# Kernel tuning notes

Measured on AMD Instinct MI355X. Metric: run time of the kernel, lower is better.

## Reference

```python
import jax, jax.numpy as jnp
import numpy as np

B, S, H, P2 = 64, 512, 768, 46  # batch, seq, hidden, num_p*2


def setup_inputs() -> dict:
    key = jax.random.key(0)
    k1, k2, k3, k4 = jax.random.split(key, 4)
    hidden_states = jax.random.normal(k1, (B, S, H), dtype=jnp.float32)
    # subject start/end indices must lie within the valid (masked-in) prefix
    lengths = jax.random.randint(k2, (B,), S // 4, S + 1)  # cue lengths per sample
    input_mask = (jnp.arange(S)[None, :] < lengths[:, None]).astype(jnp.int32)
    ids = jax.random.randint(k3, (B, 2), 0, S // 4)
    batch_subject_ids = jnp.sort(ids, axis=1).astype(jnp.int32)
    W = jax.random.normal(k4, (P2, H), dtype=jnp.float32) * (1.0 / np.sqrt(H))
    b = jnp.zeros((P2,), dtype=jnp.float32)
    return {"hidden_states": hidden_states, "batch_subject_ids": batch_subject_ids,
            "input_mask": input_mask, "W": W, "b": b}


def reference(hidden_states, batch_subject_ids, input_mask, W, b):
    # per-sample subject embedding: h[b, start] + h[b, end]  -> [B, H]
    batch_idx = jnp.arange(hidden_states.shape[0])
    s = (hidden_states[batch_idx, batch_subject_ids[:, 0]]
         + hidden_states[batch_idx, batch_subject_ids[:, 1]])
    # broadcast-add s to the first cue_len positions of each sample
    cue_len = jnp.sum(input_mask, axis=1)  # [B]
    pos_mask = (jnp.arange(hidden_states.shape[1])[None, :] < cue_len[:, None])  # [B, S]
    h = hidden_states + s[:, None, :] * pos_mask[:, :, None].astype(hidden_states.dtype)
    # linear + sigmoid^4 (dropout is identity in eval mode)
    logits = jnp.einsum('bsh,ph->bsp', h, W) + b
    return jax.nn.sigmoid(logits) ** 4
```

## Files before the change

### kernel.cpp

```cpp
#include <hip/hip_runtime.h>

#define SEQ 512
#define HID 768
#define P2  46
#define BLK 256
#define KH  384
#define WST 392

typedef short bf16x8 __attribute__((ext_vector_type(8)));
typedef float f32x4  __attribute__((ext_vector_type(4)));

__device__ __forceinline__ unsigned short f2bf(float f) {
  union { float f; unsigned int u; } v; v.f = f;
  return (unsigned short)((v.u + 0x7FFFu + ((v.u >> 16) & 1u)) >> 16);
}

__global__ __launch_bounds__(64) void qk_kernel(const float* __restrict__ h,
                                                const int* __restrict__ ids,
                                                const float* __restrict__ W,
                                                float* __restrict__ q) {
  int b = blockIdx.x, p = blockIdx.y;
  int lane = threadIdx.x;
  int i0 = ids[b * 2 + 0], i1 = ids[b * 2 + 1];
  const float* r0 = h + ((size_t)b * SEQ + i0) * HID;
  const float* r1 = h + ((size_t)b * SEQ + i1) * HID;
  const float* w  = W + (size_t)p * HID;
  float acc = 0.f;
  #pragma unroll
  for (int j = 0; j < HID / 64; ++j) {
    int k = lane + j * 64;
    acc += (r0[k] + r1[k]) * w[k];
  }
  #pragma unroll
  for (int off = 32; off > 0; off >>= 1)
    acc += __shfl_down(acc, off, 64);
  if (lane == 0) q[b * P2 + p] = acc;
}

__global__ __launch_bounds__(BLK) void gemm_kernel(const float* __restrict__ h,
                                                   const int* __restrict__ mask,
                                                   const float* __restrict__ W,
                                                   const float* __restrict__ bias,
                                                   const float* __restrict__ q,
                                                   float* __restrict__ out) {
  __shared__ __align__(16) unsigned short wlds[48 * WST];

  const int tid  = threadIdx.x;
  const int lane = tid & 63, wv = tid >> 6;
  const int mr   = lane & 15, qd = lane >> 4;
  const int row0 = blockIdx.x * 64;
  const int b    = row0 >> 9;
  const int rowa = row0 + (wv << 4) + mr;
  const float* hrow = h + (size_t)rowa * HID + (qd << 3);

  f32x4 acc[3];
  #pragma unroll
  for (int nt = 0; nt < 3; ++nt) acc[nt] = f32x4{0.f, 0.f, 0.f, 0.f};

  auto stageW = [&](int half) {
    for (int i = tid; i < (2 * WST) / 2; i += BLK)
      ((unsigned int*)(wlds + 46 * WST))[i] = 0u;
    for (int i = tid; i < (P2 * KH) / 4; i += BLK) {
      int f = i * 4;
      int r = f / KH;
      int c = f - r * KH;
      float4 w4 = *(const float4*)(W + (size_t)r * HID + half * KH + c);
      ushort4 v;
      v.x = f2bf(w4.x); v.y = f2bf(w4.y); v.z = f2bf(w4.z); v.w = f2bf(w4.w);
      *(ushort4*)&wlds[r * WST + c] = v;
    }
  };

  auto phase = [&](int half) {
    const float* hb = hrow + half * KH;
    float4 abuf[24];
    #pragma unroll
    for (int i = 0; i < 24; ++i)
      abuf[i] = *(const float4*)(hb + (i >> 1) * 32 + (i & 1) * 4);
    #pragma unroll
    for (int it = 0; it < 12; ++it) {
      bf16x8 a;
      {
        float4 x0 = abuf[2 * it], x1 = abuf[2 * it + 1];
        a[0] = (short)f2bf(x0.x); a[1] = (short)f2bf(x0.y);
        a[2] = (short)f2bf(x0.z); a[3] = (short)f2bf(x0.w);
        a[4] = (short)f2bf(x1.x); a[5] = (short)f2bf(x1.y);
        a[6] = (short)f2bf(x1.z); a[7] = (short)f2bf(x1.w);
      }
      #pragma unroll
      for (int nt = 0; nt < 3; ++nt) {
        bf16x8 bb = *(const bf16x8*)&wlds[((nt << 4) + mr) * WST + it * 32 + (qd << 3)];
        acc[nt] = __builtin_amdgcn_mfma_f32_16x16x32_bf16(a, bb, acc[nt], 0, 0, 0);
      }
    }
  };

  stageW(0);
  __syncthreads();
  phase(0);
  __syncthreads();
  stageW(1);
  __syncthreads();
  phase(1);

  int mrow[4];
  #pragma unroll
  for (int i = 0; i < 4; ++i)
    mrow[i] = mask[row0 + (wv << 4) + (qd << 2) + i];

  #pragma unroll
  for (int nt = 0; nt < 3; ++nt) {
    int p = (nt << 4) + mr;
    if (p < P2) {
      float bv = bias[p];
      float qv = q[b * P2 + p];
      #pragma unroll
      for (int i = 0; i < 4; ++i) {
        int row = row0 + (wv << 4) + (qd << 2) + i;
        float x = acc[nt][i] + bv + (mrow[i] ? qv : 0.f);
        float sg = 1.f / (1.f + __expf(-x));
        sg *= sg; sg *= sg;
        out[(size_t)row * P2 + p] = sg;
      }
    }
  }
}

extern "C" void kernel_launch(void* const* d_in, const int* in_sizes, int n_in,
                              void* d_out, int out_size, void* d_ws, size_t ws_size,
                              hipStream_t stream) {
  const float* h    = (const float*)d_in[0];
  const int*   ids  = (const int*)d_in[1];
  const int*   mask = (const int*)d_in[2];
  const float* W    = (const float*)d_in[3];
  const float* bias = (const float*)d_in[4];
  float* out = (float*)d_out;
  float* q   = (float*)d_ws;

  qk_kernel<<<dim3(64, P2), 64, 0, stream>>>(h, ids, W, q);
  gemm_kernel<<<dim3((64 * SEQ) / 64), BLK, 0, stream>>>(h, mask, W, bias, q, out);
}
```

Measured before the change: 168.0 us.

## Fuse subject-projection kernel into GEMM and stage full W once in LDS

The separate qk kernel is removed. Each GEMM block now recomputes the per-sample subject projection q (s·W) itself, using LDS and a 4-lane reduction, so one launch and the global round-trip for q go away. The full 768-wide bf16 W is staged into LDS in a single pass, which drops the two-phase staging and its extra barriers. In exchange, all 512 blocks redo the q dot products and the W conversion, and LDS use roughly doubles to about 75KB per block, which may lower occupancy.

Measured after the change: 179.7 us. +6.9%, slower.

```diff
diff --git a/kernel.cpp b/kernel.cpp
--- a/kernel.cpp
+++ b/kernel.cpp
@@ -4,8 +4,7 @@
 #define HID 768
 #define P2  46
 #define BLK 256
-#define KH  384
-#define WST 392
+#define WST 776
 
 typedef short bf16x8 __attribute__((ext_vector_type(8)));
 typedef float f32x4  __attribute__((ext_vector_type(4)));
@@ -15,35 +14,15 @@
   return (unsigned short)((v.u + 0x7FFFu + ((v.u >> 16) & 1u)) >> 16);
 }
 
-__global__ __launch_bounds__(64) void qk_kernel(const float* __restrict__ h,
-                                                const int* __restrict__ ids,
-                                                const float* __restrict__ W,
-                                                float* __restrict__ q) {
-  int b = blockIdx.x, p = blockIdx.y;
-  int lane = threadIdx.x;
-  int i0 = ids[b * 2 + 0], i1 = ids[b * 2 + 1];
-  const float* r0 = h + ((size_t)b * SEQ + i0) * HID;
-  const float* r1 = h + ((size_t)b * SEQ + i1) * HID;
-  const float* w  = W + (size_t)p * HID;
-  float acc = 0.f;
-  #pragma unroll
-  for (int j = 0; j < HID / 64; ++j) {
-    int k = lane + j * 64;
-    acc += (r0[k] + r1[k]) * w[k];
-  }
-  #pragma unroll
-  for (int off = 32; off > 0; off >>= 1)
-    acc += __shfl_down(acc, off, 64);
-  if (lane == 0) q[b * P2 + p] = acc;
-}
-
-__global__ __launch_bounds__(BLK) void gemm_kernel(const float* __restrict__ h,
-                                                   const int* __restrict__ mask,
-                                                   const float* __restrict__ W,
-                                                   const float* __restrict__ bias,
-                                                   const float* __restrict__ q,
-                                                   float* __restrict__ out) {
+__global__ __launch_bounds__(BLK) void fused_kernel(const float* __restrict__ h,
+                                                    const int* __restrict__ ids,
+                                                    const int* __restrict__ mask,
+                                                    const float* __restrict__ W,
+                                                    const float* __restrict__ bias,
+                                                    float* __restrict__ out) {
   __shared__ __align__(16) unsigned short wlds[48 * WST];
+  __shared__ __align__(16) float s_lds[HID];
+  __shared__ float q_lds[48];
 
   const int tid  = threadIdx.x;
   const int lane = tid & 63, wv = tid >> 6;
@@ -53,26 +32,53 @@
   const int rowa = row0 + (wv << 4) + mr;
   const float* hrow = h + (size_t)rowa * HID + (qd << 3);
 
+  for (int i = tid; i < WST; i += BLK)
+    ((unsigned int*)(wlds + 46 * WST))[i] = 0u;
+  for (int i = tid; i < (P2 * HID) / 4; i += BLK) {
+    int f = i * 4;
+    int r = f / HID;
+    int c = f - r * HID;
+    float4 w4 = *(const float4*)(W + (size_t)r * HID + c);
+    ushort4 v;
+    v.x = f2bf(w4.x); v.y = f2bf(w4.y); v.z = f2bf(w4.z); v.w = f2bf(w4.w);
+    *(ushort4*)&wlds[r * WST + c] = v;
+  }
+  {
+    int i0 = ids[b * 2 + 0], i1 = ids[b * 2 + 1];
+    const float* r0 = h + ((size_t)b * SEQ + i0) * HID;
+    const float* r1 = h + ((size_t)b * SEQ + i1) * HID;
+    #pragma unroll
+    for (int j = 0; j < HID / BLK; ++j) {
+      int k = tid + j * BLK;
+      s_lds[k] = r0[k] + r1[k];
+    }
+  }
+  __syncthreads();
+
+  if (tid < P2 * 4) {
+    int p = tid >> 2, kq = tid & 3;
+    const float4* wp = (const float4*)(W + (size_t)p * HID + kq * 192);
+    float acc = 0.f;
+    #pragma unroll 8
+    for (int j = 0; j < 48; ++j) {
+      float4 w4 = wp[j];
+      int k = kq * 192 + j * 4;
+      acc += s_lds[k] * w4.x + s_lds[k + 1] * w4.y
+           + s_lds[k + 2] * w4.z + s_lds[k + 3] * w4.w;
+    }
+    acc += __shfl_xor(acc, 1, 64);
+    acc += __shfl_xor(acc, 2, 64);
+    if (kq == 0) q_lds[p] = acc;
+  }
+  __syncthreads();
+
   f32x4 acc[3];
   #pragma unroll
   for (int nt = 0; nt < 3; ++nt) acc[nt] = f32x4{0.f, 0.f, 0.f, 0.f};
 
-  auto stageW = [&](int half) {
-    for (int i = tid; i < (2 * WST) / 2; i += BLK)
-      ((unsigned int*)(wlds + 46 * WST))[i] = 0u;
-    for (int i = tid; i < (P2 * KH) / 4; i += BLK) {
-      int f = i * 4;
-      int r = f / KH;
-      int c = f - r * KH;
-      float4 w4 = *(const float4*)(W + (size_t)r * HID + half * KH + c);
-      ushort4 v;
-      v.x = f2bf(w4.x); v.y = f2bf(w4.y); v.z = f2bf(w4.z); v.w = f2bf(w4.w);
-      *(ushort4*)&wlds[r * WST + c] = v;
-    }
-  };
-
-  auto phase = [&](int half) {
-    const float* hb = hrow + half * KH;
+  #pragma unroll
+  for (int half = 0; half < 2; ++half) {
+    const float* hb = hrow + half * 384;
     float4 abuf[24];
     #pragma unroll
     for (int i = 0; i < 24; ++i)
@@ -89,19 +95,12 @@
       }
       #pragma unroll
       for (int nt = 0; nt < 3; ++nt) {
-        bf16x8 bb = *(const bf16x8*)&wlds[((nt << 4) + mr) * WST + it * 32 + (qd << 3)];
+        bf16x8 bb = *(const bf16x8*)&wlds[((nt << 4) + mr) * WST
+                                          + half * 384 + it * 32 + (qd << 3)];
         acc[nt] = __builtin_amdgcn_mfma_f32_16x16x32_bf16(a, bb, acc[nt], 0, 0, 0);
       }
     }
-  };
-
-  stageW(0);
-  __syncthreads();
-  phase(0);
-  __syncthreads();
-  stageW(1);
-  __syncthreads();
-  phase(1);
+  }
 
   int mrow[4];
   #pragma unroll
@@ -113,7 +112,7 @@
     int p = (nt << 4) + mr;
     if (p < P2) {
       float bv = bias[p];
-      float qv = q[b * P2 + p];
+      float qv = q_lds[p];
       #pragma unroll
       for (int i = 0; i < 4; ++i) {
         int row = row0 + (wv << 4) + (qd << 2) + i;
@@ -135,8 +134,6 @@
   const float* W    = (const float*)d_in[3];
   const float* bias = (const float*)d_in[4];
   float* out = (float*)d_out;
-  float* q   = (float*)d_ws;
 
-  qk_kernel<<<dim3(64, P2), 64, 0, stream>>>(h, ids, W, q);
-  gemm_kernel<<<dim3((64 * SEQ) / 64), BLK, 0, stream>>>(h, mask, W, bias, q, out);
+  fused_kernel<<<dim3((64 * SEQ) / 64), BLK, 0, stream>>>(h, ids, mask, W, bias, out);
 }
```
